# Optimization experiments

Hardware: AMD Instinct MI355X
Metric: run time of the kernel (lower is better)

The kernel has to match this reference:

```python
import jax, jax.numpy as jnp
import numpy as np

DIM = 768
HEADS = 12
DH = DIM // HEADS
HIDDEN = 4 * DIM
EPS = 1e-5


def layernorm(x, g, b):
    mu = jnp.mean(x, axis=-1, keepdims=True)
    var = jnp.mean(jnp.square(x - mu), axis=-1, keepdims=True)
    return (x - mu) * jax.lax.rsqrt(var + EPS) * g + b


def setup_inputs() -> dict:
    key = jax.random.key(0)
    ks = jax.random.split(key, 12)
    B, N = 8, 1024
    s_in = 1.0 / np.sqrt(DIM)
    s_hid = 1.0 / np.sqrt(HIDDEN)
    return {
        "x": jax.random.normal(ks[0], (B, N, DIM), jnp.float32),
        "q_extra": jax.random.normal(ks[1], (B, N, DIM), jnp.float32),
        "ln1_g": jnp.ones((DIM,), jnp.float32),
        "ln1_b": jnp.zeros((DIM,), jnp.float32),
        "w_kv": jax.random.normal(ks[2], (DIM, 2 * DIM), jnp.float32) * s_in,
        "w_out": jax.random.normal(ks[3], (DIM, DIM), jnp.float32) * s_in,
        "b_out": jnp.zeros((DIM,), jnp.float32),
        "ln2_g": jnp.ones((DIM,), jnp.float32),
        "ln2_b": jnp.zeros((DIM,), jnp.float32),
        "w1": jax.random.normal(ks[4], (DIM, HIDDEN), jnp.float32) * s_in,
        "b1": jnp.zeros((HIDDEN,), jnp.float32),
        "w2": jax.random.normal(ks[5], (HIDDEN, DIM), jnp.float32) * s_hid,
        "b2": jnp.zeros((DIM,), jnp.float32),
    }


def reference(x, q_extra, ln1_g, ln1_b, w_kv, w_out, b_out, ln2_g, ln2_b, w1, b1, w2, b2):
    B, N, C = x.shape
    scale = DH ** (-0.5)

    # pre-norm cross attention
    xn = layernorm(x, ln1_g, ln1_b)
    kv = (xn @ w_kv).reshape(B, N, 2, HEADS, DH)
    k = kv[:, :, 0]  # [B,N,H,Dh]
    v = kv[:, :, 1]
    q = q_extra.reshape(B, N, HEADS, DH)
    dots = jnp.einsum('bnhd,bmhd->bhnm', q, k) * scale
    attn = jax.nn.softmax(dots, axis=-1)
    out = jnp.einsum('bhnm,bmhd->bnhd', attn, v).reshape(B, N, C)
    out = out @ w_out + b_out

    x = x + out  # residual

    # pre-norm MLP
    h = layernorm(x, ln2_g, ln2_b)
    h = jax.nn.gelu(h @ w1 + b1, approximate=False)
    h = h @ w2 + b2
    return x + h
```

## Files before the change

### kernel.cpp

```cpp
#include <hip/hip_runtime.h>
#include <math.h>

typedef __attribute__((ext_vector_type(8))) short short8;
typedef __attribute__((ext_vector_type(8))) _Float16 half8;
typedef __attribute__((ext_vector_type(2))) __fp16 fp16x2;
typedef __attribute__((ext_vector_type(4))) float float4v;

__device__ __forceinline__ unsigned short f2bf(float f) {
  union { unsigned int i; float f; } x; x.f = f;
  unsigned int r = x.i + 0x7fffu + ((x.i >> 16) & 1u);
  return (unsigned short)(r >> 16);
}

__global__ void ln_kernel(const float* __restrict__ in, const float* __restrict__ g,
                          const float* __restrict__ b, unsigned short* __restrict__ out) {
  const int row = blockIdx.x, t = threadIdx.x;
  const float* xr = in + (size_t)row * 768;
  float v0 = xr[t], v1 = xr[t + 256], v2 = xr[t + 512];
  float s = v0 + v1 + v2;
  float s2 = v0 * v0 + v1 * v1 + v2 * v2;
  for (int off = 32; off > 0; off >>= 1) {
    s += __shfl_xor(s, off, 64);
    s2 += __shfl_xor(s2, off, 64);
  }
  __shared__ float red[8];
  const int wave = t >> 6, lane = t & 63;
  if (lane == 0) { red[wave] = s; red[wave + 4] = s2; }
  __syncthreads();
  s = red[0] + red[1] + red[2] + red[3];
  s2 = red[4] + red[5] + red[6] + red[7];
  const float mu = s * (1.0f / 768.0f);
  const float var = s2 * (1.0f / 768.0f) - mu * mu;
  const float rstd = rsqrtf(var + 1e-5f);
  unsigned short* orow = out + (size_t)row * 768;
  orow[t]       = f2bf((v0 - mu) * rstd * g[t]       + b[t]);
  orow[t + 256] = f2bf((v1 - mu) * rstd * g[t + 256] + b[t + 256]);
  orow[t + 512] = f2bf((v2 - mu) * rstd * g[t + 512] + b[t + 512]);
}

__global__ void wtrans_kernel(const float* __restrict__ in, unsigned short* __restrict__ out,
                              int K, int N) {
  __shared__ float tile[32][33];
  const int k0 = blockIdx.y * 32, n0 = blockIdx.x * 32;
  const int tr = threadIdx.x >> 5, tc = threadIdx.x & 31;
#pragma unroll
  for (int i = 0; i < 4; ++i)
    tile[tr + i * 8][tc] = in[(size_t)(k0 + tr + i * 8) * N + n0 + tc];
  __syncthreads();
#pragma unroll
  for (int i = 0; i < 4; ++i)
    out[(size_t)(n0 + tr + i * 8) * K + k0 + tc] = f2bf(tile[tc][tr + i * 8]);
}

#define SWIZ_BLOCK(GX, TW)                                        \
  const int _id = (int)blockIdx.x;                                \
  const int _gy8 = (int)gridDim.x / (8 * (GX));                   \
  const int _xcd = _id & 7, _jj = _id >> 3;                       \
  const int row0 = (_xcd * _gy8 + _jj / (GX)) * 128;              \
  const int col0 = (_jj % (GX)) * (TW);

__device__ __forceinline__ void gemm128(
    const unsigned short* __restrict__ A, int lda,
    const unsigned short* __restrict__ Bt, int ldb, int K,
    int row0, int col0,
    unsigned short* As, unsigned short* Bs,
    float4v acc[4][4]) {
  const int t = threadIdx.x, lane = t & 63, wave = t >> 6;
  const int quad = lane >> 4, l16 = lane & 15;
  const int wr = wave >> 1, wc = wave & 1;
  const int srow = lane >> 3;
  const int scol = ((lane & 7) ^ srow) * 8;
#pragma unroll
  for (int mt = 0; mt < 4; ++mt)
#pragma unroll
    for (int nt = 0; nt < 4; ++nt) acc[mt][nt] = (float4v)(0.0f);

  for (int kk = 0; kk < K; kk += 64) {
    __syncthreads();
#pragma unroll
    for (int j = 0; j < 4; ++j) {
      const int chunk = wave * 4 + j;
      const int r = chunk * 8 + srow;
      __builtin_amdgcn_global_load_lds(
          (const __attribute__((address_space(1))) unsigned int*)(A + (size_t)(row0 + r) * lda + kk + scol),
          (__attribute__((address_space(3))) unsigned int*)(As + chunk * 512),
          16, 0, 0);
      __builtin_amdgcn_global_load_lds(
          (const __attribute__((address_space(1))) unsigned int*)(Bt + (size_t)(col0 + r) * ldb + kk + scol),
          (__attribute__((address_space(3))) unsigned int*)(Bs + chunk * 512),
          16, 0, 0);
    }
    __syncthreads();
#pragma unroll
    for (int ks = 0; ks < 2; ++ks) {
      const int gsw = ((ks * 4 + quad) ^ (l16 & 7)) * 8;
      short8 af[4], bfv[4];
#pragma unroll
      for (int i = 0; i < 4; ++i) {
        af[i]  = *(const short8*)(As + (wr * 64 + i * 16 + l16) * 64 + gsw);
        bfv[i] = *(const short8*)(Bs + (wc * 64 + i * 16 + l16) * 64 + gsw);
      }
#pragma unroll
      for (int mt = 0; mt < 4; ++mt)
#pragma unroll
        for (int nt = 0; nt < 4; ++nt)
          acc[mt][nt] = __builtin_amdgcn_mfma_f32_16x16x32_bf16(af[mt], bfv[nt], acc[mt][nt], 0, 0, 0);
    }
  }
}

#define GEMM128_PROLOGUE(GX)                                     \
  __shared__ unsigned short As[128 * 64];                        \
  __shared__ unsigned short Bs[128 * 64];                        \
  float4v acc[4][4];                                             \
  SWIZ_BLOCK(GX, 128)                                            \
  const int t = threadIdx.x, lane = t & 63, wave = t >> 6;       \
  const int quad = lane >> 4, l16 = lane & 15;                   \
  const int wr = wave >> 1, wc = wave & 1; (void)t;

__device__ __forceinline__ void gemm12864(
    const unsigned short* __restrict__ A, int lda,
    const unsigned short* __restrict__ Bt, int ldb, int K,
    int row0, int col0,
    unsigned short* As, unsigned short* Bs,
    float4v acc[2][4]) {
  const int t = threadIdx.x, lane = t & 63, wave = t >> 6;
  const int quad = lane >> 4, l16 = lane & 15;
  const int srow = lane >> 3;
  const int scol = ((lane & 7) ^ srow) * 8;
#pragma unroll
  for (int mt = 0; mt < 2; ++mt)
#pragma unroll
    for (int nt = 0; nt < 4; ++nt) acc[mt][nt] = (float4v)(0.0f);

  for (int kk = 0; kk < K; kk += 64) {
    __syncthreads();
#pragma unroll
    for (int j = 0; j < 4; ++j) {
      const int chunk = wave * 4 + j;
      const int r = chunk * 8 + srow;
      __builtin_amdgcn_global_load_lds(
          (const __attribute__((address_space(1))) unsigned int*)(A + (size_t)(row0 + r) * lda + kk + scol),
          (__attribute__((address_space(3))) unsigned int*)(As + chunk * 512),
          16, 0, 0);
    }
#pragma unroll
    for (int j = 0; j < 2; ++j) {
      const int chunk = wave * 2 + j;
      const int r = chunk * 8 + srow;
      __builtin_amdgcn_global_load_lds(
          (const __attribute__((address_space(1))) unsigned int*)(Bt + (size_t)(col0 + r) * ldb + kk + scol),
          (__attribute__((address_space(3))) unsigned int*)(Bs + chunk * 512),
          16, 0, 0);
    }
    __syncthreads();
#pragma unroll
    for (int ks = 0; ks < 2; ++ks) {
      const int gsw = ((ks * 4 + quad) ^ (l16 & 7)) * 8;
      short8 af[2], bfv[4];
#pragma unroll
      for (int i = 0; i < 2; ++i)
        af[i] = *(const short8*)(As + (wave * 32 + i * 16 + l16) * 64 + gsw);
#pragma unroll
      for (int i = 0; i < 4; ++i)
        bfv[i] = *(const short8*)(Bs + (i * 16 + l16) * 64 + gsw);
#pragma unroll
      for (int mt = 0; mt < 2; ++mt)
#pragma unroll
        for (int nt = 0; nt < 4; ++nt)
          acc[mt][nt] = __builtin_amdgcn_mfma_f32_16x16x32_bf16(af[mt], bfv[nt], acc[mt][nt], 0, 0, 0);
    }
  }
}

#define GEMM12864_PROLOGUE(GX)                                   \
  __shared__ unsigned short As[128 * 64];                        \
  __shared__ unsigned short Bs[64 * 64];                         \
  float4v acc[2][4];                                             \
  SWIZ_BLOCK(GX, 64)                                             \
  const int t = threadIdx.x, lane = t & 63, wave = t >> 6;       \
  const int quad = lane >> 4, l16 = lane & 15; (void)t;

__global__ void gemm_kv_kernel(const unsigned short* __restrict__ xn,
                               const unsigned short* __restrict__ wkvt,
                               _Float16* __restrict__ kbuf,
                               _Float16* __restrict__ vtbuf) {
  GEMM128_PROLOGUE(12)
  gemm128(xn, 768, wkvt, 768, 768, row0, col0, As, Bs, acc);
#pragma unroll
  for (int mt = 0; mt < 4; ++mt)
#pragma unroll
    for (int nt = 0; nt < 4; ++nt) {
      const int j = col0 + wc * 64 + nt * 16 + l16;
#pragma unroll
      for (int r = 0; r < 4; ++r) {
        const int m = row0 + wr * 64 + mt * 16 + quad * 4 + r;
        const int bb = m >> 10, n = m & 1023;
        const float c = acc[mt][nt][r];
        if (j < 768) {
          const int hh = j >> 6, d = j & 63;
          kbuf[((size_t)(bb * 12 + hh) * 1024 + n) * 64 + d] = (_Float16)c;
        } else {
          const int j2 = j - 768, hh = j2 >> 6, d = j2 & 63;
          vtbuf[((size_t)(bb * 12 + hh) * 64 + d) * 1024 + n] = (_Float16)c;
        }
      }
    }
}

#define AST 72
#define PST 72
__global__ void attn_kernel(const float* __restrict__ q_extra,
                            const _Float16* __restrict__ kbuf,
                            const _Float16* __restrict__ vtbuf,
                            unsigned short* __restrict__ ao) {
  __shared__ _Float16 Ks[64 * AST];
  __shared__ _Float16 Vs[64 * AST];
  __shared__ _Float16 Ps[4][16 * PST];
  const int id = (int)blockIdx.x;
  const int pair = id % 96, qb = id / 96;
  const int h = pair >> 3, b = pair & 7;
  const int q0 = qb * 64;
  const int t = threadIdx.x, lane = t & 63, wave = t >> 6;
  const int quad = lane >> 4, l16 = lane & 15;

  const float QS = 0.125f * 1.44269504088896f;
  half8 qf0, qf1;
  {
    const float* qp = q_extra +
        ((size_t)((b * 1024 + q0 + wave * 16 + l16) * 12 + h)) * 64 + quad * 8;
    float4 a0 = *(const float4*)(qp);
    float4 a1 = *(const float4*)(qp + 4);
    float4 c0 = *(const float4*)(qp + 32);
    float4 c1 = *(const float4*)(qp + 36);
    union { fp16x2 h2[4]; half8 h8; } u0, u1;
    u0.h2[0] = __builtin_amdgcn_cvt_pkrtz(a0.x * QS, a0.y * QS);
    u0.h2[1] = __builtin_amdgcn_cvt_pkrtz(a0.z * QS, a0.w * QS);
    u0.h2[2] = __builtin_amdgcn_cvt_pkrtz(a1.x * QS, a1.y * QS);
    u0.h2[3] = __builtin_amdgcn_cvt_pkrtz(a1.z * QS, a1.w * QS);
    u1.h2[0] = __builtin_amdgcn_cvt_pkrtz(c0.x * QS, c0.y * QS);
    u1.h2[1] = __builtin_amdgcn_cvt_pkrtz(c0.z * QS, c0.w * QS);
    u1.h2[2] = __builtin_amdgcn_cvt_pkrtz(c1.x * QS, c1.y * QS);
    u1.h2[3] = __builtin_amdgcn_cvt_pkrtz(c1.z * QS, c1.w * QS);
    qf0 = u0.h8; qf1 = u1.h8;
  }

  const _Float16* kb = kbuf + (size_t)(b * 12 + h) * 65536;
  const _Float16* vb = vtbuf + (size_t)(b * 12 + h) * 65536;
  const int srow = t >> 2, su = (t & 3) * 16;

  half8 kp0 = *(const half8*)(kb + (size_t)srow * 64 + su);
  half8 kp1 = *(const half8*)(kb + (size_t)srow * 64 + su + 8);
  half8 vp0 = *(const half8*)(vb + (size_t)srow * 1024 + su);
  half8 vp1 = *(const half8*)(vb + (size_t)srow * 1024 + su + 8);

  float m_s = -1e30f, l_s = 0.0f;
  float4v acc[4];
  acc[0] = (float4v)(0.f); acc[1] = (float4v)(0.f);
  acc[2] = (float4v)(0.f); acc[3] = (float4v)(0.f);
  _Float16* pw = Ps[wave];

  for (int c = 0; c < 16; ++c) {
    __syncthreads();
    *(half8*)(Ks + srow * AST + su)     = kp0;
    *(half8*)(Ks + srow * AST + su + 8) = kp1;
    *(half8*)(Vs + srow * AST + su)     = vp0;
    *(half8*)(Vs + srow * AST + su + 8) = vp1;
    if (c < 15) {
      const int key1 = (c + 1) * 64;
      kp0 = *(const half8*)(kb + (size_t)(key1 + srow) * 64 + su);
      kp1 = *(const half8*)(kb + (size_t)(key1 + srow) * 64 + su + 8);
      vp0 = *(const half8*)(vb + (size_t)srow * 1024 + key1 + su);
      vp1 = *(const half8*)(vb + (size_t)srow * 1024 + key1 + su + 8);
    }
    __syncthreads();

    float4v s[4];
#pragma unroll
    for (int kt = 0; kt < 4; ++kt) {
      const _Float16* kr = Ks + (kt * 16 + l16) * AST;
      half8 kf0 = *(const half8*)(kr + quad * 8);
      half8 kf1 = *(const half8*)(kr + 32 + quad * 8);
      float4v a = (float4v)(0.f);
      a = __builtin_amdgcn_mfma_f32_16x16x32_f16(kf0, qf0, a, 0, 0, 0);
      a = __builtin_amdgcn_mfma_f32_16x16x32_f16(kf1, qf1, a, 0, 0, 0);
      s[kt] = a;
    }

    float mx = fmaxf(fmaxf(fmaxf(s[0][0], s[0][1]), fmaxf(s[0][2], s[0][3])),
                     fmaxf(fmaxf(s[1][0], s[1][1]), fmaxf(s[1][2], s[1][3])));
    mx = fmaxf(mx, fmaxf(fmaxf(fmaxf(s[2][0], s[2][1]), fmaxf(s[2][2], s[2][3])),
                         fmaxf(fmaxf(s[3][0], s[3][1]), fmaxf(s[3][2], s[3][3]))));
    mx = fmaxf(mx, __shfl_xor(mx, 16, 64));
    mx = fmaxf(mx, __shfl_xor(mx, 32, 64));
    const float mn = fmaxf(m_s, mx);
    const float alpha = exp2f(m_s - mn);
    m_s = mn;

    float sum = 0.0f;
#pragma unroll
    for (int kt = 0; kt < 4; ++kt) {
      const float p0 = exp2f(s[kt][0] - mn);
      const float p1 = exp2f(s[kt][1] - mn);
      const float p2 = exp2f(s[kt][2] - mn);
      const float p3 = exp2f(s[kt][3] - mn);
      sum += (p0 + p1) + (p2 + p3);
      union { fp16x2 h2[2]; uint2 u; } pk;
      pk.h2[0] = __builtin_amdgcn_cvt_pkrtz(p0, p1);
      pk.h2[1] = __builtin_amdgcn_cvt_pkrtz(p2, p3);
      *(uint2*)(pw + l16 * PST + kt * 16 + quad * 4) = pk.u;
    }
    sum += __shfl_xor(sum, 16, 64);
    sum += __shfl_xor(sum, 32, 64);
    l_s = l_s * alpha + sum;

    float ab[4];
#pragma unroll
    for (int r = 0; r < 4; ++r) ab[r] = __shfl(alpha, quad * 4 + r, 64);
#pragma unroll
    for (int nt = 0; nt < 4; ++nt)
#pragma unroll
      for (int r = 0; r < 4; ++r) acc[nt][r] *= ab[r];

    half8 pf0 = *(const half8*)(pw + l16 * PST + quad * 8);
    half8 pf1 = *(const half8*)(pw + l16 * PST + 32 + quad * 8);
#pragma unroll
    for (int nt = 0; nt < 4; ++nt) {
      const _Float16* vr = Vs + (nt * 16 + l16) * AST;
      half8 vf0 = *(const half8*)(vr + quad * 8);
      half8 vf1 = *(const half8*)(vr + 32 + quad * 8);
      acc[nt] = __builtin_amdgcn_mfma_f32_16x16x32_f16(pf0, vf0, acc[nt], 0, 0, 0);
      acc[nt] = __builtin_amdgcn_mfma_f32_16x16x32_f16(pf1, vf1, acc[nt], 0, 0, 0);
    }
  }

  const float inv = 1.0f / l_s;
  float ib[4];
#pragma unroll
  for (int r = 0; r < 4; ++r) ib[r] = __shfl(inv, quad * 4 + r, 64);
#pragma unroll
  for (int nt = 0; nt < 4; ++nt) {
#pragma unroll
    for (int r = 0; r < 4; ++r) {
      const int m = q0 + wave * 16 + quad * 4 + r;
      ao[(size_t)(b * 1024 + m) * 768 + h * 64 + nt * 16 + l16] =
          f2bf(acc[nt][r] * ib[r]);
    }
  }
}

__global__ void gemm_outproj_kernel(const unsigned short* __restrict__ ao,
                                    const unsigned short* __restrict__ woutt,
                                    const float* __restrict__ b_out,
                                    const float* __restrict__ x,
                                    float* __restrict__ x2) {
  GEMM12864_PROLOGUE(12)
  gemm12864(ao, 768, woutt, 768, 768, row0, col0, As, Bs, acc);
#pragma unroll
  for (int mt = 0; mt < 2; ++mt)
#pragma unroll
    for (int nt = 0; nt < 4; ++nt) {
      const int j = col0 + nt * 16 + l16;
#pragma unroll
      for (int r = 0; r < 4; ++r) {
        const int m = row0 + wave * 32 + mt * 16 + quad * 4 + r;
        const size_t idx = (size_t)m * 768 + j;
        x2[idx] = acc[mt][nt][r] + b_out[j] + x[idx];
      }
    }
}

__global__ void gemm_mlp1_kernel(const unsigned short* __restrict__ h,
                                 const unsigned short* __restrict__ w1t,
                                 const float* __restrict__ b1,
                                 unsigned short* __restrict__ h1) {
  GEMM128_PROLOGUE(24)
  gemm128(h, 768, w1t, 768, 768, row0, col0, As, Bs, acc);
#pragma unroll
  for (int mt = 0; mt < 4; ++mt)
#pragma unroll
    for (int nt = 0; nt < 4; ++nt) {
      const int j = col0 + wc * 64 + nt * 16 + l16;
#pragma unroll
      for (int r = 0; r < 4; ++r) {
        const int m = row0 + wr * 64 + mt * 16 + quad * 4 + r;
        const float y = acc[mt][nt][r] + b1[j];
        const float ge = 0.5f * y * (1.0f + erff(y * 0.70710678118654752f));
        h1[(size_t)m * 3072 + j] = f2bf(ge);
      }
    }
}

__global__ void gemm_mlp2_kernel(const unsigned short* __restrict__ h1,
                                 const unsigned short* __restrict__ w2t,
                                 const float* __restrict__ b2,
                                 const float* __restrict__ x2,
                                 float* __restrict__ out) {
  GEMM12864_PROLOGUE(12)
  gemm12864(h1, 3072, w2t, 3072, 3072, row0, col0, As, Bs, acc);
#pragma unroll
  for (int mt = 0; mt < 2; ++mt)
#pragma unroll
    for (int nt = 0; nt < 4; ++nt) {
      const int j = col0 + nt * 16 + l16;
#pragma unroll
      for (int r = 0; r < 4; ++r) {
        const int m = row0 + wave * 32 + mt * 16 + quad * 4 + r;
        const size_t idx = (size_t)m * 768 + j;
        out[idx] = acc[mt][nt][r] + b2[j] + x2[idx];
      }
    }
}

extern "C" void kernel_launch(void* const* d_in, const int* in_sizes, int n_in,
                              void* d_out, int out_size, void* d_ws, size_t ws_size,
                              hipStream_t stream) {
  const float* x       = (const float*)d_in[0];
  const float* q_extra = (const float*)d_in[1];
  const float* ln1_g   = (const float*)d_in[2];
  const float* ln1_b   = (const float*)d_in[3];
  const float* w_kv    = (const float*)d_in[4];
  const float* w_out   = (const float*)d_in[5];
  const float* b_out   = (const float*)d_in[6];
  const float* ln2_g   = (const float*)d_in[7];
  const float* ln2_b   = (const float*)d_in[8];
  const float* w1      = (const float*)d_in[9];
  const float* b1      = (const float*)d_in[10];
  const float* w2      = (const float*)d_in[11];
  const float* b2      = (const float*)d_in[12];
  float* out = (float*)d_out;

  char* ws = (char*)d_ws;
  unsigned short* xn    = (unsigned short*)(ws);
  _Float16*       kbuf  = (_Float16*)(ws + 12582912);
  _Float16*       vtbuf = (_Float16*)(ws + 25165824);
  unsigned short* ao    = (unsigned short*)(ws + 37748736);
  float*          x2    = (float*)(ws + 50331648);
  unsigned short* h1    = (unsigned short*)(ws + 75497472);
  unsigned short* hbuf  = xn;
  unsigned short* wkvt  = ao;
  unsigned short* woutt = h1;
  unsigned short* w1t   = (unsigned short*)kbuf;
  unsigned short* w2t   = (unsigned short*)vtbuf;

  ln_kernel<<<8192, 256, 0, stream>>>(x, ln1_g, ln1_b, xn);
  wtrans_kernel<<<dim3(48, 24), 256, 0, stream>>>(w_kv, wkvt, 768, 1536);
  wtrans_kernel<<<dim3(24, 24), 256, 0, stream>>>(w_out, woutt, 768, 768);
  gemm_kv_kernel<<<768, 256, 0, stream>>>(xn, wkvt, kbuf, vtbuf);
  attn_kernel<<<1536, 256, 0, stream>>>(q_extra, kbuf, vtbuf, ao);
  wtrans_kernel<<<dim3(96, 24), 256, 0, stream>>>(w1, w1t, 768, 3072);
  wtrans_kernel<<<dim3(24, 96), 256, 0, stream>>>(w2, w2t, 3072, 768);
  gemm_outproj_kernel<<<768, 256, 0, stream>>>(ao, woutt, b_out, x, x2);
  ln_kernel<<<8192, 256, 0, stream>>>(x2, ln2_g, ln2_b, hbuf);
  gemm_mlp1_kernel<<<1536, 256, 0, stream>>>(hbuf, w1t, b1, h1);
  gemm_mlp2_kernel<<<768, 256, 0, stream>>>(h1, w2t, b2, x2, out);
}
```

Before: 379.5 us.

## Process two query sub-tiles per wave in attention and skip small rescales

Each attention block now covers 128 queries instead of 64, with each wave handling two 16-row query sub-tiles against the same K/V tile in shared memory. This halves the grid and the K/V global loads and LDS staging per query. A lazy-rescale test skips the alpha rescale of the accumulators when the new max exceeds the running max by no more than 8 (log2 units), and a launch-bounds hint of 3 blocks per CU is added. The cost is more registers per wave, fewer blocks for the GPU to schedule, and fp16 probabilities that can reach up to 256 before normalization.

```diff
diff --git a/kernel.cpp b/kernel.cpp
--- a/kernel.cpp
+++ b/kernel.cpp
@@ -210,25 +210,27 @@
 
 #define AST 72
 #define PST 72
-__global__ void attn_kernel(const float* __restrict__ q_extra,
-                            const _Float16* __restrict__ kbuf,
-                            const _Float16* __restrict__ vtbuf,
-                            unsigned short* __restrict__ ao) {
+__global__ __launch_bounds__(256, 3)
+void attn_kernel(const float* __restrict__ q_extra,
+                 const _Float16* __restrict__ kbuf,
+                 const _Float16* __restrict__ vtbuf,
+                 unsigned short* __restrict__ ao) {
   __shared__ _Float16 Ks[64 * AST];
   __shared__ _Float16 Vs[64 * AST];
-  __shared__ _Float16 Ps[4][16 * PST];
+  __shared__ _Float16 Ps[4][2][16 * PST];
   const int id = (int)blockIdx.x;
   const int pair = id % 96, qb = id / 96;
   const int h = pair >> 3, b = pair & 7;
-  const int q0 = qb * 64;
+  const int q0 = qb * 128;
   const int t = threadIdx.x, lane = t & 63, wave = t >> 6;
   const int quad = lane >> 4, l16 = lane & 15;
 
   const float QS = 0.125f * 1.44269504088896f;
-  half8 qf0, qf1;
-  {
+  half8 qf[2][2];
+#pragma unroll
+  for (int qs = 0; qs < 2; ++qs) {
     const float* qp = q_extra +
-        ((size_t)((b * 1024 + q0 + wave * 16 + l16) * 12 + h)) * 64 + quad * 8;
+        ((size_t)((b * 1024 + q0 + wave * 32 + qs * 16 + l16) * 12 + h)) * 64 + quad * 8;
     float4 a0 = *(const float4*)(qp);
     float4 a1 = *(const float4*)(qp + 4);
     float4 c0 = *(const float4*)(qp + 32);
@@ -242,7 +244,7 @@
     u1.h2[1] = __builtin_amdgcn_cvt_pkrtz(c0.z * QS, c0.w * QS);
     u1.h2[2] = __builtin_amdgcn_cvt_pkrtz(c1.x * QS, c1.y * QS);
     u1.h2[3] = __builtin_amdgcn_cvt_pkrtz(c1.z * QS, c1.w * QS);
-    qf0 = u0.h8; qf1 = u1.h8;
+    qf[qs][0] = u0.h8; qf[qs][1] = u1.h8;
   }
 
   const _Float16* kb = kbuf + (size_t)(b * 12 + h) * 65536;
@@ -254,11 +256,12 @@
   half8 vp0 = *(const half8*)(vb + (size_t)srow * 1024 + su);
   half8 vp1 = *(const half8*)(vb + (size_t)srow * 1024 + su + 8);
 
-  float m_s = -1e30f, l_s = 0.0f;
-  float4v acc[4];
-  acc[0] = (float4v)(0.f); acc[1] = (float4v)(0.f);
-  acc[2] = (float4v)(0.f); acc[3] = (float4v)(0.f);
-  _Float16* pw = Ps[wave];
+  float m_s[2] = {-1e30f, -1e30f}, l_s[2] = {0.0f, 0.0f};
+  float4v acc[2][4];
+#pragma unroll
+  for (int qs = 0; qs < 2; ++qs)
+#pragma unroll
+    for (int nt = 0; nt < 4; ++nt) acc[qs][nt] = (float4v)(0.0f);
 
   for (int c = 0; c < 16; ++c) {
     __syncthreads();
@@ -275,76 +278,86 @@
     }
     __syncthreads();
 
-    float4v s[4];
-#pragma unroll
-    for (int kt = 0; kt < 4; ++kt) {
-      const _Float16* kr = Ks + (kt * 16 + l16) * AST;
-      half8 kf0 = *(const half8*)(kr + quad * 8);
-      half8 kf1 = *(const half8*)(kr + 32 + quad * 8);
-      float4v a = (float4v)(0.f);
-      a = __builtin_amdgcn_mfma_f32_16x16x32_f16(kf0, qf0, a, 0, 0, 0);
-      a = __builtin_amdgcn_mfma_f32_16x16x32_f16(kf1, qf1, a, 0, 0, 0);
-      s[kt] = a;
-    }
-
-    float mx = fmaxf(fmaxf(fmaxf(s[0][0], s[0][1]), fmaxf(s[0][2], s[0][3])),
-                     fmaxf(fmaxf(s[1][0], s[1][1]), fmaxf(s[1][2], s[1][3])));
-    mx = fmaxf(mx, fmaxf(fmaxf(fmaxf(s[2][0], s[2][1]), fmaxf(s[2][2], s[2][3])),
-                         fmaxf(fmaxf(s[3][0], s[3][1]), fmaxf(s[3][2], s[3][3]))));
-    mx = fmaxf(mx, __shfl_xor(mx, 16, 64));
-    mx = fmaxf(mx, __shfl_xor(mx, 32, 64));
-    const float mn = fmaxf(m_s, mx);
-    const float alpha = exp2f(m_s - mn);
-    m_s = mn;
-
-    float sum = 0.0f;
-#pragma unroll
-    for (int kt = 0; kt < 4; ++kt) {
-      const float p0 = exp2f(s[kt][0] - mn);
-      const float p1 = exp2f(s[kt][1] - mn);
-      const float p2 = exp2f(s[kt][2] - mn);
-      const float p3 = exp2f(s[kt][3] - mn);
-      sum += (p0 + p1) + (p2 + p3);
-      union { fp16x2 h2[2]; uint2 u; } pk;
-      pk.h2[0] = __builtin_amdgcn_cvt_pkrtz(p0, p1);
-      pk.h2[1] = __builtin_amdgcn_cvt_pkrtz(p2, p3);
-      *(uint2*)(pw + l16 * PST + kt * 16 + quad * 4) = pk.u;
-    }
-    sum += __shfl_xor(sum, 16, 64);
-    sum += __shfl_xor(sum, 32, 64);
-    l_s = l_s * alpha + sum;
-
-    float ab[4];
-#pragma unroll
-    for (int r = 0; r < 4; ++r) ab[r] = __shfl(alpha, quad * 4 + r, 64);
-#pragma unroll
-    for (int nt = 0; nt < 4; ++nt)
-#pragma unroll
-      for (int r = 0; r < 4; ++r) acc[nt][r] *= ab[r];
-
-    half8 pf0 = *(const half8*)(pw + l16 * PST + quad * 8);
-    half8 pf1 = *(const half8*)(pw + l16 * PST + 32 + quad * 8);
+#pragma unroll
+    for (int qs = 0; qs < 2; ++qs) {
+      float4v s[4];
+#pragma unroll
+      for (int kt = 0; kt < 4; ++kt) {
+        const _Float16* kr = Ks + (kt * 16 + l16) * AST;
+        half8 kf0 = *(const half8*)(kr + quad * 8);
+        half8 kf1 = *(const half8*)(kr + 32 + quad * 8);
+        float4v a = (float4v)(0.f);
+        a = __builtin_amdgcn_mfma_f32_16x16x32_f16(kf0, qf[qs][0], a, 0, 0, 0);
+        a = __builtin_amdgcn_mfma_f32_16x16x32_f16(kf1, qf[qs][1], a, 0, 0, 0);
+        s[kt] = a;
+      }
+
+      float mx = fmaxf(fmaxf(fmaxf(s[0][0], s[0][1]), fmaxf(s[0][2], s[0][3])),
+                       fmaxf(fmaxf(s[1][0], s[1][1]), fmaxf(s[1][2], s[1][3])));
+      mx = fmaxf(mx, fmaxf(fmaxf(fmaxf(s[2][0], s[2][1]), fmaxf(s[2][2], s[2][3])),
+                           fmaxf(fmaxf(s[3][0], s[3][1]), fmaxf(s[3][2], s[3][3]))));
+      mx = fmaxf(mx, __shfl_xor(mx, 16, 64));
+      mx = fmaxf(mx, __shfl_xor(mx, 32, 64));
+
+      if (!__all(mx <= m_s[qs] + 8.0f)) {
+        const float mn = fmaxf(m_s[qs], mx);
+        const float alpha = exp2f(m_s[qs] - mn);
+        m_s[qs] = mn;
+        l_s[qs] *= alpha;
+        float ab[4];
+#pragma unroll
+        for (int r = 0; r < 4; ++r) ab[r] = __shfl(alpha, quad * 4 + r, 64);
+#pragma unroll
+        for (int nt = 0; nt < 4; ++nt)
+#pragma unroll
+          for (int r = 0; r < 4; ++r) acc[qs][nt][r] *= ab[r];
+      }
+
+      _Float16* pw = Ps[wave][qs];
+      float sum = 0.0f;
+#pragma unroll
+      for (int kt = 0; kt < 4; ++kt) {
+        const float p0 = exp2f(s[kt][0] - m_s[qs]);
+        const float p1 = exp2f(s[kt][1] - m_s[qs]);
+        const float p2 = exp2f(s[kt][2] - m_s[qs]);
+        const float p3 = exp2f(s[kt][3] - m_s[qs]);
+        sum += (p0 + p1) + (p2 + p3);
+        union { fp16x2 h2[2]; uint2 u; } pk;
+        pk.h2[0] = __builtin_amdgcn_cvt_pkrtz(p0, p1);
+        pk.h2[1] = __builtin_amdgcn_cvt_pkrtz(p2, p3);
+        *(uint2*)(pw + l16 * PST + kt * 16 + quad * 4) = pk.u;
+      }
+      sum += __shfl_xor(sum, 16, 64);
+      sum += __shfl_xor(sum, 32, 64);
+      l_s[qs] += sum;
+
+      half8 pf0 = *(const half8*)(pw + l16 * PST + quad * 8);
+      half8 pf1 = *(const half8*)(pw + l16 * PST + 32 + quad * 8);
+#pragma unroll
+      for (int nt = 0; nt < 4; ++nt) {
+        const _Float16* vr = Vs + (nt * 16 + l16) * AST;
+        half8 vf0 = *(const half8*)(vr + quad * 8);
+        half8 vf1 = *(const half8*)(vr + 32 + quad * 8);
+        acc[qs][nt] = __builtin_amdgcn_mfma_f32_16x16x32_f16(pf0, vf0, acc[qs][nt], 0, 0, 0);
+        acc[qs][nt] = __builtin_amdgcn_mfma_f32_16x16x32_f16(pf1, vf1, acc[qs][nt], 0, 0, 0);
+      }
+    }
+  }
+
+#pragma unroll
+  for (int qs = 0; qs < 2; ++qs) {
+    const float inv = 1.0f / l_s[qs];
+    float ib[4];
+#pragma unroll
+    for (int r = 0; r < 4; ++r) ib[r] = __shfl(inv, quad * 4 + r, 64);
 #pragma unroll
     for (int nt = 0; nt < 4; ++nt) {
-      const _Float16* vr = Vs + (nt * 16 + l16) * AST;
-      half8 vf0 = *(const half8*)(vr + quad * 8);
-      half8 vf1 = *(const half8*)(vr + 32 + quad * 8);
-      acc[nt] = __builtin_amdgcn_mfma_f32_16x16x32_f16(pf0, vf0, acc[nt], 0, 0, 0);
-      acc[nt] = __builtin_amdgcn_mfma_f32_16x16x32_f16(pf1, vf1, acc[nt], 0, 0, 0);
-    }
-  }
-
-  const float inv = 1.0f / l_s;
-  float ib[4];
-#pragma unroll
-  for (int r = 0; r < 4; ++r) ib[r] = __shfl(inv, quad * 4 + r, 64);
-#pragma unroll
-  for (int nt = 0; nt < 4; ++nt) {
-#pragma unroll
-    for (int r = 0; r < 4; ++r) {
-      const int m = q0 + wave * 16 + quad * 4 + r;
-      ao[(size_t)(b * 1024 + m) * 768 + h * 64 + nt * 16 + l16] =
-          f2bf(acc[nt][r] * ib[r]);
+#pragma unroll
+      for (int r = 0; r < 4; ++r) {
+        const int m = q0 + wave * 32 + qs * 16 + quad * 4 + r;
+        ao[(size_t)(b * 1024 + m) * 768 + h * 64 + nt * 16 + l16] =
+            f2bf(acc[qs][nt][r] * ib[r]);
+      }
     }
   }
 }
@@ -447,7 +460,7 @@
   wtrans_kernel<<<dim3(48, 24), 256, 0, stream>>>(w_kv, wkvt, 768, 1536);
   wtrans_kernel<<<dim3(24, 24), 256, 0, stream>>>(w_out, woutt, 768, 768);
   gemm_kv_kernel<<<768, 256, 0, stream>>>(xn, wkvt, kbuf, vtbuf);
-  attn_kernel<<<1536, 256, 0, stream>>>(q_extra, kbuf, vtbuf, ao);
+  attn_kernel<<<768, 256, 0, stream>>>(q_extra, kbuf, vtbuf, ao);
   wtrans_kernel<<<dim3(96, 24), 256, 0, stream>>>(w1, w1t, 768, 3072);
   wtrans_kernel<<<dim3(24, 96), 256, 0, stream>>>(w2, w2t, 3072, 768);
   gemm_outproj_kernel<<<768, 256, 0, stream>>>(ao, woutt, b_out, x, x2);
```

New measurement: 382.6 us. About the same (+0.8%).
